# Kernel tuning notes

Measured on AMD Instinct MI355X. Metric: run time of the kernel, lower is better.

The kernel has to match this reference:

```python
import jax, jax.numpy as jnp
import numpy as np

W0, W1, W2 = 1.0, 1e-4, 1e-5  # loss_weight


def _gray_mask(imgs):
    """Emulate ToPILImage -> convert('L') -> mean-threshold point() -> ToTensor.
    imgs: [B,3,H,W] float in [0,1]. Returns binary mask in {0,1}, broadcast to [B,3,H,W].
    """
    u8 = jnp.floor(imgs * 255.0)  # ToPILImage: mul(255).byte() truncation
    # PIL L-mode: (R*299 + G*587 + B*114) / 1000, integer truncated
    gray = jnp.floor((u8[:, 0] * 299.0 + u8[:, 1] * 587.0 + u8[:, 2] * 114.0) / 1000.0)
    thres = gray.mean(axis=(1, 2), keepdims=True)  # np.array(mask).mean() per sample
    mask = jnp.where(gray > thres, 0.0, 1.0)       # point(0 if x>thres else 255) then /255
    return jnp.broadcast_to(mask[:, None], imgs.shape)


def _gradient_map(x):
    # finite-difference gradient magnitude with zero-padded shifts
    B, C, H, W = x.shape
    r = jnp.pad(x, ((0, 0), (0, 0), (0, 0), (0, 1)))[..., 1:]       # x[j+1], 0 at right edge
    l = jnp.pad(x, ((0, 0), (0, 0), (0, 0), (1, 0)))[..., :W]       # x[j-1], 0 at left edge
    t = jnp.pad(x, ((0, 0), (0, 0), (1, 0), (0, 0)))[..., :H, :]    # x[i-1], 0 at top edge
    b = jnp.pad(x, ((0, 0), (0, 0), (0, 1), (0, 0)))[..., 1:, :]    # x[i+1], 0 at bottom edge
    return jnp.sqrt(((r - l) * 0.5) ** 2 + ((t - b) * 0.5) ** 2 + 1e-6)


def setup_inputs() -> dict:
    key = jax.random.key(0)
    k1, k2, k3, k4 = jax.random.split(key, 4)
    return {
        "out_images": jax.random.uniform(k1, (128, 3, 128, 512), dtype=jnp.float32),
        "target_images": jax.random.uniform(k2, (128, 3, 128, 512), dtype=jnp.float32),
        "text_pred": jax.random.normal(k3, (4096, 10000), dtype=jnp.float32),
        "text_gt": jax.random.randint(k4, (4096,), 0, 10000, dtype=jnp.int64),
    }


def reference(out_images, target_images, text_pred, text_gt):
    # l2: MSE over images
    l2 = jnp.mean((out_images - target_images) ** 2)
    # lg: L1 between gradient maps of binarized masks (masks are detached: built via PIL)
    mo = jax.lax.stop_gradient(_gray_mask(out_images))
    mt = jax.lax.stop_gradient(_gray_mask(target_images))
    lg = jnp.mean(jnp.abs(_gradient_map(mo) - _gradient_map(mt)))
    # lce: mean cross-entropy
    logp = jax.nn.log_softmax(text_pred, axis=-1)
    ce = -jnp.mean(jnp.take_along_axis(logp, text_gt[:, None], axis=-1))
    return W0 * l2 + W1 * lg + W2 * ce
```

## Files before the change

kernel.cpp:

```cpp
#include <hip/hip_runtime.h>
#include <hip/hip_bf16.h>
#include <math.h>

#define BB 128
#define HH 128
#define WW 512
#define HW (HH*WW)
#define NPIX ((size_t)BB*HW)
#define ROWS 4096
#define COLS 10000
#define P1_BLOCKS (BB*16)
#define LCE_BLOCKS (ROWS/4)
#define GRID (P1_BLOCKS + LCE_BLOCKS)


__device__ __forceinline__ int gray_of(float r, float g, float b) {
    int ri = (int)floorf(r * 255.0f);
    int gi = (int)floorf(g * 255.0f);
    int bi = (int)floorf(b * 255.0f);
    return (299 * ri + 587 * gi + 114 * bi) / 1000;
}

__device__ __forceinline__ float e4(float4 x) {
    return (__expf(x.x) + __expf(x.y)) + (__expf(x.z) + __expf(x.w));
}

template <bool STORE_GRAY>
__global__ __launch_bounds__(256) void fused1_kernel(
    const float* __restrict__ outI, const float* __restrict__ tgtI,
    const float* __restrict__ X, const int* __restrict__ gt,
    float* __restrict__ l2p, int* __restrict__ gso, int* __restrict__ gst,
    float* __restrict__ cep,
    unsigned char* __restrict__ gout, unsigned char* __restrict__ gtgt) {
    const int tid = threadIdx.x;
    const int bid = blockIdx.x;
    const int wid = tid >> 6, lane = tid & 63;

    if ((bid % 3) != 2) {
        const int p1    = 2 * (bid / 3) + (bid % 3);
        const int b     = p1 >> 4;
        const int chunk = p1 & 15;
        const float4* o4 = (const float4*)(outI + (size_t)b * 3 * HW) + chunk * 1024;
        const float4* t4 = (const float4*)(tgtI + (size_t)b * 3 * HW) + chunk * 1024;
        uchar4* go4 = (uchar4*)(gout + (size_t)b * HW) + chunk * 1024;
        uchar4* gt4 = (uchar4*)(gtgt + (size_t)b * HW) + chunk * 1024;

        float4 o[12], t[12];
#pragma unroll
        for (int k = 0; k < 4; ++k) {
            int v = tid + k * 256;
            o[3*k+0] = o4[v]; o[3*k+1] = o4[v + HW/4]; o[3*k+2] = o4[v + 2*(HW/4)];
        }
#pragma unroll
        for (int k = 0; k < 4; ++k) {
            int v = tid + k * 256;
            t[3*k+0] = t4[v]; t[3*k+1] = t4[v + HW/4]; t[3*k+2] = t4[v + 2*(HW/4)];
        }

        float l2 = 0.0f;
        int so = 0, st = 0;
#pragma unroll
        for (int k = 0; k < 4; ++k) {
            float4 oR = o[3*k], oG = o[3*k+1], oB = o[3*k+2];
            float4 tR = t[3*k], tG = t[3*k+1], tB = t[3*k+2];
            float d;
            d = oR.x-tR.x; l2 += d*d;  d = oR.y-tR.y; l2 += d*d;
            d = oR.z-tR.z; l2 += d*d;  d = oR.w-tR.w; l2 += d*d;
            d = oG.x-tG.x; l2 += d*d;  d = oG.y-tG.y; l2 += d*d;
            d = oG.z-tG.z; l2 += d*d;  d = oG.w-tG.w; l2 += d*d;
            d = oB.x-tB.x; l2 += d*d;  d = oB.y-tB.y; l2 += d*d;
            d = oB.z-tB.z; l2 += d*d;  d = oB.w-tB.w; l2 += d*d;

            int g0 = gray_of(oR.x, oG.x, oB.x);
            int g1 = gray_of(oR.y, oG.y, oB.y);
            int g2 = gray_of(oR.z, oG.z, oB.z);
            int g3 = gray_of(oR.w, oG.w, oB.w);
            so += g0 + g1 + g2 + g3;
            if (STORE_GRAY) go4[tid + k*256] = make_uchar4((unsigned char)g0,(unsigned char)g1,(unsigned char)g2,(unsigned char)g3);
            g0 = gray_of(tR.x, tG.x, tB.x);
            g1 = gray_of(tR.y, tG.y, tB.y);
            g2 = gray_of(tR.z, tG.z, tB.z);
            g3 = gray_of(tR.w, tG.w, tB.w);
            st += g0 + g1 + g2 + g3;
            if (STORE_GRAY) gt4[tid + k*256] = make_uchar4((unsigned char)g0,(unsigned char)g1,(unsigned char)g2,(unsigned char)g3);
        }

        for (int off = 32; off > 0; off >>= 1) {
            l2 += __shfl_down(l2, off);
            so += __shfl_down(so, off);
            st += __shfl_down(st, off);
        }
        __shared__ float wl2[4];
        __shared__ int w1[4], w2[4];
        if (lane == 0) { wl2[wid] = l2; w1[wid] = so; w2[wid] = st; }
        __syncthreads();
        if (tid == 0) {
            l2p[p1] = wl2[0] + wl2[1] + wl2[2] + wl2[3];
            gso[p1] = w1[0] + w1[1] + w1[2] + w1[3];
            gst[p1] = w2[0] + w2[1] + w2[2] + w2[3];
        }
    } else {
        const int row = (bid / 3) * 4 + wid;
        const float4* xr = (const float4*)(X + (size_t)row * COLS);

        float s = 0.0f;
        int v = lane;
#pragma unroll
        for (int k = 0; k < 9; ++k, v += 256) {
            float4 a = xr[v], b2 = xr[v+64], c = xr[v+128], d = xr[v+192];
            s += e4(a) + e4(b2) + e4(c) + e4(d);
        }
        {
            float4 a = xr[v], b2 = xr[v+64], c = xr[v+128];
            s += e4(a) + e4(b2) + e4(c);
            if (v + 192 < COLS/4) s += e4(xr[v+192]);
        }
        for (int off = 32; off > 0; off >>= 1) s += __shfl_down(s, off);
        if (lane == 0) {
            float xg = X[(size_t)row * COLS + gt[row]];
            cep[row] = __logf(s) - xg;
        }
    }
}

__device__ __forceinline__ int mask8(uint2 v, int ti) {
    int m = 0;
#pragma unroll
    for (int k = 0; k < 4; ++k) m |= (((int)((v.x >> (8*k)) & 255) <= ti) ? 1 : 0) << k;
#pragma unroll
    for (int k = 0; k < 4; ++k) m |= (((int)((v.y >> (8*k)) & 255) <= ti) ? 1 : 0) << (k+4);
    return m;
}

__device__ __forceinline__ void grad_bits(const unsigned char* __restrict__ G,
                                          int r, int roff, int ti, int lane,
                                          int& ax, int& vy) {
    uint2 cc = *(const uint2*)(G + roff);
    uint2 aa = *(const uint2*)(G + (r > 0   ? roff - 512 : roff));
    uint2 bb = *(const uint2*)(G + (r < 127 ? roff + 512 : roff));
    int mc = mask8(cc, ti);
    int ma = (r > 0)   ? mask8(aa, ti) : 0;
    int mb = (r < 127) ? mask8(bb, ti) : 0;
    int prev = __shfl_up(mc, 1);
    int next = __shfl_down(mc, 1);
    int lb = ((mc << 1) & 0xFF) | ((lane > 0)  ? ((prev >> 7) & 1) : 0);
    int rb = (mc >> 1)          | ((lane < 63) ? ((next & 1) << 7) : 0);
    ax = lb ^ rb;
    vy = ma ^ mb;
}

__global__ __launch_bounds__(256) void pass2_kernel(
    const unsigned char* __restrict__ gout, const unsigned char* __restrict__ gtgt,
    const int* __restrict__ gso, const int* __restrict__ gst,
    float* __restrict__ lgp) {
    const int tid  = threadIdx.x;
    const int wave = tid >> 6, lane = tid & 63;
    const int b  = blockIdx.x >> 4;
    const int rg = blockIdx.x & 15;

    int s_o = 0, s_t = 0;
#pragma unroll
    for (int k = 0; k < 16; ++k) { s_o += gso[b*16 + k]; s_t += gst[b*16 + k]; }
    const int ti_o = s_o >> 16;
    const int ti_t = s_t >> 16;
    const unsigned char* Go = gout + (size_t)b * HW;
    const unsigned char* Gt = gtgt + (size_t)b * HW;

    const float v0 = sqrtf(1e-6f);
    const float v1 = sqrtf(0.25f + 1e-6f);
    const float v2 = sqrtf(0.5f + 1e-6f);

    float sum = 0.0f;
#pragma unroll
    for (int rr = 0; rr < 2; ++rr) {
        const int r = rg * 8 + wave * 2 + rr;
        const int roff = r * 512 + lane * 8;
        int ax_o, vy_o, ax_t, vy_t;
        grad_bits(Go, r, roff, ti_o, lane, ax_o, vy_o);
        grad_bits(Gt, r, roff, ti_t, lane, ax_t, vy_t);
#pragma unroll
        for (int k = 0; k < 8; ++k) {
            int so = ((ax_o >> k) & 1) + ((vy_o >> k) & 1);
            int st = ((ax_t >> k) & 1) + ((vy_t >> k) & 1);
            float g_o = (so == 0) ? v0 : ((so == 1) ? v1 : v2);
            float g_t = (st == 0) ? v0 : ((st == 1) ? v1 : v2);
            sum += fabsf(g_o - g_t);
        }
    }

    for (int off = 32; off > 0; off >>= 1) sum += __shfl_down(sum, off);
    __shared__ float ws4[4];
    if (lane == 0) ws4[wave] = sum;
    __syncthreads();
    if (tid == 0) lgp[blockIdx.x] = ws4[0] + ws4[1] + ws4[2] + ws4[3];
}

__device__ __forceinline__ float mask_at(const float* __restrict__ img, size_t base, int p, float thres) {
    float r = img[base + p], g = img[base + p + HW], b = img[base + p + 2*HW];
    return ((float)gray_of(r, g, b) > thres) ? 0.0f : 1.0f;
}

__global__ __launch_bounds__(256) void pass2_recompute_kernel(
    const float* __restrict__ outI, const float* __restrict__ tgtI,
    const int* __restrict__ gso, const int* __restrict__ gst,
    float* __restrict__ lgp) {
    const int tid   = threadIdx.x;
    const int b     = blockIdx.x >> 4;
    const int chunk = blockIdx.x & 15;
    int s_o = 0, s_t = 0;
    for (int k = 0; k < 16; ++k) { s_o += gso[b*16 + k]; s_t += gst[b*16 + k]; }
    const float to = (float)s_o * (1.0f/65536.0f);
    const float tt = (float)s_t * (1.0f/65536.0f);
    const size_t baseO = (size_t)b * 3 * HW;

    float sum = 0.0f;
    for (int u = 0; u < 16; ++u) {
        int p = chunk * 4096 + u * 256 + tid;
        int i = p >> 9, j = p & 511;
        float mr = (j+1 < WW) ? mask_at(outI, baseO, p+1,  to) : 0.0f;
        float ml = (j-1 >= 0) ? mask_at(outI, baseO, p-1,  to) : 0.0f;
        float mt = (i-1 >= 0) ? mask_at(outI, baseO, p-WW, to) : 0.0f;
        float mb = (i+1 < HH) ? mask_at(outI, baseO, p+WW, to) : 0.0f;
        float dx = (mr - ml) * 0.5f, dy = (mt - mb) * 0.5f;
        float gmo = sqrtf(dx*dx + dy*dy + 1e-6f);
        mr = (j+1 < WW) ? mask_at(tgtI, baseO, p+1,  tt) : 0.0f;
        ml = (j-1 >= 0) ? mask_at(tgtI, baseO, p-1,  tt) : 0.0f;
        mt = (i-1 >= 0) ? mask_at(tgtI, baseO, p-WW, tt) : 0.0f;
        mb = (i+1 < HH) ? mask_at(tgtI, baseO, p+WW, tt) : 0.0f;
        dx = (mr - ml) * 0.5f; dy = (mt - mb) * 0.5f;
        float gmt = sqrtf(dx*dx + dy*dy + 1e-6f);
        sum += fabsf(gmo - gmt);
    }

    __shared__ float sred[256];
    sred[tid] = sum;
    __syncthreads();
    for (int off = 128; off > 0; off >>= 1) {
        if (tid < off) sred[tid] += sred[tid+off];
        __syncthreads();
    }
    if (tid == 0) lgp[blockIdx.x] = sred[0];
}

__global__ __launch_bounds__(256) void combine_kernel(
    const float* __restrict__ l2p, const float* __restrict__ lgp,
    const float* __restrict__ cep, float* __restrict__ out) {
    __shared__ double s0[256], s1[256], s2[256];
    const int t = threadIdx.x;
    double a = 0.0, bsum = 0.0, c = 0.0;
    for (int i = t; i < 2048; i += 256) { a += (double)l2p[i]; bsum += (double)lgp[i]; }
    for (int i = t; i < 4096; i += 256) c += (double)cep[i];
    s0[t] = a; s1[t] = bsum; s2[t] = c;
    __syncthreads();
    for (int off = 128; off > 0; off >>= 1) {
        if (t < off) { s0[t] += s0[t+off]; s1[t] += s1[t+off]; s2[t] += s2[t+off]; }
        __syncthreads();
    }
    if (t == 0) {
        double l2 = s0[0] / (double)(3.0 * (double)NPIX);
        double lg = s1[0] / (double)NPIX;
        double ce = s2[0] / (double)ROWS;
        out[0] = (float)(l2 + 1e-4 * lg + 1e-5 * ce);
    }
}

extern "C" void kernel_launch(void* const* d_in, const int* in_sizes, int n_in,
                              void* d_out, int out_size, void* d_ws, size_t ws_size,
                              hipStream_t stream) {
    const float* outI = (const float*)d_in[0];
    const float* tgtI = (const float*)d_in[1];
    const float* X    = (const float*)d_in[2];
    const int*   gt   = (const int*)d_in[3];

    float* l2p = (float*)d_ws;
    int*   gso = (int*)((char*)d_ws + 8192);
    int*   gst = (int*)((char*)d_ws + 16384);
    float* lgp = (float*)((char*)d_ws + 24576);
    float* cep = (float*)((char*)d_ws + 32768);
    unsigned char* gray = (unsigned char*)d_ws + 65536;
    const size_t need = 65536 + 2 * NPIX;
    const bool useCache = ws_size >= need;

    if (useCache) {
        fused1_kernel<true><<<GRID, 256, 0, stream>>>(
            outI, tgtI, X, gt, l2p, gso, gst, cep, gray, gray + NPIX);
        pass2_kernel<<<BB * 16, 256, 0, stream>>>(gray, gray + NPIX, gso, gst, lgp);
    } else {
        fused1_kernel<false><<<GRID, 256, 0, stream>>>(
            outI, tgtI, X, gt, l2p, gso, gst, cep, gray, gray);
        pass2_recompute_kernel<<<BB * 16, 256, 0, stream>>>(outI, tgtI, gso, gst, lgp);
    }
    combine_kernel<<<1, 256, 0, stream>>>(l2p, lgp, cep, (float*)d_out);
}
```

Measured before the change: 98.18 us.

## Split cross-entropy rows across two waves and interleave blocks evenly

Each softmax row is now split into two halves, each handled by its own wavefront. Partial exp sums go to the workspace and the final log and subtraction move into the combine kernel. The block interleave changes from 2:1 image-to-CE to 1:1, and image loads are merged into one loop behind a scheduling barrier with a launch-bounds occupancy hint. The aim is to balance the fused grid and expose more memory parallelism, at the cost of an extra workspace round-trip and more blocks.

```diff
diff --git a/kernel.cpp b/kernel.cpp
--- a/kernel.cpp
+++ b/kernel.cpp
@@ -10,7 +10,7 @@
 #define ROWS 4096
 #define COLS 10000
 #define P1_BLOCKS (BB*16)
-#define LCE_BLOCKS (ROWS/4)
+#define LCE_BLOCKS 2048
 #define GRID (P1_BLOCKS + LCE_BLOCKS)
 
 
@@ -26,18 +26,18 @@
 }
 
 template <bool STORE_GRAY>
-__global__ __launch_bounds__(256) void fused1_kernel(
+__global__ __launch_bounds__(256, 2) void fused1_kernel(
     const float* __restrict__ outI, const float* __restrict__ tgtI,
     const float* __restrict__ X, const int* __restrict__ gt,
     float* __restrict__ l2p, int* __restrict__ gso, int* __restrict__ gst,
-    float* __restrict__ cep,
+    float* __restrict__ cesp, float* __restrict__ xgp,
     unsigned char* __restrict__ gout, unsigned char* __restrict__ gtgt) {
     const int tid = threadIdx.x;
     const int bid = blockIdx.x;
     const int wid = tid >> 6, lane = tid & 63;
 
-    if ((bid % 3) != 2) {
-        const int p1    = 2 * (bid / 3) + (bid % 3);
+    if ((bid & 1) == 0) {
+        const int p1    = bid >> 1;
         const int b     = p1 >> 4;
         const int chunk = p1 & 15;
         const float4* o4 = (const float4*)(outI + (size_t)b * 3 * HW) + chunk * 1024;
@@ -50,12 +50,9 @@
         for (int k = 0; k < 4; ++k) {
             int v = tid + k * 256;
             o[3*k+0] = o4[v]; o[3*k+1] = o4[v + HW/4]; o[3*k+2] = o4[v + 2*(HW/4)];
-        }
-#pragma unroll
-        for (int k = 0; k < 4; ++k) {
-            int v = tid + k * 256;
             t[3*k+0] = t4[v]; t[3*k+1] = t4[v + HW/4]; t[3*k+2] = t4[v + 2*(HW/4)];
         }
+        __builtin_amdgcn_sched_barrier(0);
 
         float l2 = 0.0f;
         int so = 0, st = 0;
@@ -100,25 +97,27 @@
             gst[p1] = w2[0] + w2[1] + w2[2] + w2[3];
         }
     } else {
-        const int row = (bid / 3) * 4 + wid;
-        const float4* xr = (const float4*)(X + (size_t)row * COLS);
+        const int unit = (bid >> 1) * 4 + wid;
+        const int row  = unit >> 1;
+        const int h    = unit & 1;
+        const float4* xh = (const float4*)(X + (size_t)row * COLS) + h * 1250;
 
         float s = 0.0f;
-        int v = lane;
-#pragma unroll
-        for (int k = 0; k < 9; ++k, v += 256) {
-            float4 a = xr[v], b2 = xr[v+64], c = xr[v+128], d = xr[v+192];
+#pragma unroll
+        for (int k = 0; k < 4; ++k) {
+            int v = lane + k * 256;
+            float4 a = xh[v], b2 = xh[v+64], c = xh[v+128], d = xh[v+192];
             s += e4(a) + e4(b2) + e4(c) + e4(d);
         }
         {
-            float4 a = xr[v], b2 = xr[v+64], c = xr[v+128];
+            float4 a = xh[1024+lane], b2 = xh[1088+lane], c = xh[1152+lane];
             s += e4(a) + e4(b2) + e4(c);
-            if (v + 192 < COLS/4) s += e4(xr[v+192]);
+            if (1216 + lane < 1250) s += e4(xh[1216+lane]);
         }
         for (int off = 32; off > 0; off >>= 1) s += __shfl_down(s, off);
         if (lane == 0) {
-            float xg = X[(size_t)row * COLS + gt[row]];
-            cep[row] = __logf(s) - xg;
+            cesp[unit] = s;
+            if (h == 0) xgp[row] = X[(size_t)row * COLS + gt[row]];
         }
     }
 }
@@ -244,12 +243,14 @@
 
 __global__ __launch_bounds__(256) void combine_kernel(
     const float* __restrict__ l2p, const float* __restrict__ lgp,
-    const float* __restrict__ cep, float* __restrict__ out) {
+    const float* __restrict__ cesp, const float* __restrict__ xgp,
+    float* __restrict__ out) {
     __shared__ double s0[256], s1[256], s2[256];
     const int t = threadIdx.x;
     double a = 0.0, bsum = 0.0, c = 0.0;
     for (int i = t; i < 2048; i += 256) { a += (double)l2p[i]; bsum += (double)lgp[i]; }
-    for (int i = t; i < 4096; i += 256) c += (double)cep[i];
+    for (int i = t; i < 4096; i += 256)
+        c += (double)(__logf(cesp[2*i] + cesp[2*i+1]) - xgp[i]);
     s0[t] = a; s1[t] = bsum; s2[t] = c;
     __syncthreads();
     for (int off = 128; off > 0; off >>= 1) {
@@ -272,23 +273,24 @@
     const float* X    = (const float*)d_in[2];
     const int*   gt   = (const int*)d_in[3];
 
-    float* l2p = (float*)d_ws;
-    int*   gso = (int*)((char*)d_ws + 8192);
-    int*   gst = (int*)((char*)d_ws + 16384);
-    float* lgp = (float*)((char*)d_ws + 24576);
-    float* cep = (float*)((char*)d_ws + 32768);
-    unsigned char* gray = (unsigned char*)d_ws + 65536;
-    const size_t need = 65536 + 2 * NPIX;
+    float* l2p  = (float*)d_ws;
+    int*   gso  = (int*)((char*)d_ws + 8192);
+    int*   gst  = (int*)((char*)d_ws + 16384);
+    float* lgp  = (float*)((char*)d_ws + 24576);
+    float* cesp = (float*)((char*)d_ws + 32768);
+    float* xgp  = (float*)((char*)d_ws + 65536);
+    unsigned char* gray = (unsigned char*)d_ws + 98304;
+    const size_t need = 98304 + 2 * NPIX;
     const bool useCache = ws_size >= need;
 
     if (useCache) {
         fused1_kernel<true><<<GRID, 256, 0, stream>>>(
-            outI, tgtI, X, gt, l2p, gso, gst, cep, gray, gray + NPIX);
+            outI, tgtI, X, gt, l2p, gso, gst, cesp, xgp, gray, gray + NPIX);
         pass2_kernel<<<BB * 16, 256, 0, stream>>>(gray, gray + NPIX, gso, gst, lgp);
     } else {
         fused1_kernel<false><<<GRID, 256, 0, stream>>>(
-            outI, tgtI, X, gt, l2p, gso, gst, cep, gray, gray);
+            outI, tgtI, X, gt, l2p, gso, gst, cesp, xgp, gray, gray);
         pass2_recompute_kernel<<<BB * 16, 256, 0, stream>>>(outI, tgtI, gso, gst, lgp);
     }
-    combine_kernel<<<1, 256, 0, stream>>>(l2p, lgp, cep, (float*)d_out);
-}
+    combine_kernel<<<1, 256, 0, stream>>>(l2p, lgp, cesp, xgp, (float*)d_out);
+}
```

Result: faster. 93.48 us (-4.8%).
